# Kernel optimization log

Hardware: AMD Instinct MI355X
Metric: run time of the kernel (lower is better)

## Reference

```python
import jax, jax.numpy as jnp
import numpy as np

B, N, C, H = 2, 2048, 1024, 16
D = C // H
EPS = 1e-5  # torch LayerNorm default


def layernorm(x, gamma, beta):
    mu = jnp.mean(x, axis=-1, keepdims=True)
    var = jnp.mean(jnp.square(x - mu), axis=-1, keepdims=True)
    return (x - mu) * jax.lax.rsqrt(var + EPS) * gamma + beta


def setup_inputs() -> dict:
    key = jax.random.key(0)
    ks = jax.random.split(key, 4)
    x = jax.random.normal(ks[0], (B, N, C), dtype=jnp.float32)
    w_qkv = jax.random.normal(ks[1], (3 * C, C), dtype=jnp.float32) * (C ** -0.5)
    w_proj = jax.random.normal(ks[2], (C, C), dtype=jnp.float32) * (C ** -0.5)
    return {
        "x": x,
        "w_qkv": w_qkv,
        "q_gamma": jnp.ones((C,), jnp.float32),
        "q_beta": jnp.zeros((C,), jnp.float32),
        "k_gamma": jnp.ones((C,), jnp.float32),
        "k_beta": jnp.zeros((C,), jnp.float32),
        "lpe_w": jnp.ones((C,), jnp.float32),
        "lpe_b": jnp.zeros((C,), jnp.float32),
        "w_proj": w_proj,
        "b_proj": jnp.zeros((C,), jnp.float32),
    }


def reference(x, w_qkv, q_gamma, q_beta, k_gamma, k_beta, lpe_w, lpe_b, w_proj, b_proj):
    b, n, c = x.shape
    scale = D ** -0.5
    qkv = jnp.einsum('bnc,fc->bnf', x, w_qkv)            # (B,N,3C)
    qkv = qkv.reshape(b, n, 3, H, D)
    q, k, v = qkv[:, :, 0], qkv[:, :, 1], qkv[:, :, 2]   # (B,N,H,D)
    # QK-norm: LayerNorm over flattened heads (dim C)
    q = layernorm(q.reshape(b, n, c), q_gamma, q_beta).reshape(b, n, H, D)
    k = layernorm(k.reshape(b, n, c), k_gamma, k_beta).reshape(b, n, H, D)
    # LPE: depthwise 1x1x1 conv == per-channel affine on v
    v_lpe = v.reshape(b, n, c) * lpe_w + lpe_b           # (B,N,C)
    # attention
    attn = jnp.einsum('bqhd,bkhd->bhqk', q * scale, k)   # (B,H,N,N)
    attn = jax.nn.softmax(attn, axis=-1)
    out = jnp.einsum('bhqk,bkhd->bqhd', attn, v).reshape(b, n, c)
    y = jnp.einsum('bnc,oc->bno', out + v_lpe, w_proj) + b_proj
    return y
```

## Files before the change

kernel.cpp:

```cpp
#include <hip/hip_runtime.h>
#include <stdint.h>

#define Bdim 2
#define Ndim 2048
#define Cdim 1024
#define Hdim 16
#define Ddim 64
#define Fdim 3072
#define Mdim 4096

typedef unsigned int  u32;
typedef unsigned short u16;
typedef float f32x4 __attribute__((ext_vector_type(4)));
typedef short s16x8 __attribute__((ext_vector_type(8)));
typedef unsigned short u16x4 __attribute__((ext_vector_type(4)));
typedef unsigned int u32x2 __attribute__((ext_vector_type(2)));

__device__ __forceinline__ u16 f2b(float f) {
  u32 u = __builtin_bit_cast(u32, f);
  u += 0x7FFFu + ((u >> 16) & 1u);
  return (u16)(u >> 16);
}
__device__ __forceinline__ float b2f(u16 h) {
  return __builtin_bit_cast(float, (u32)h << 16);
}
__device__ __forceinline__ u32 cvtpk(float a, float b) {
  u32 d;
  asm("v_cvt_pk_bf16_f32 %0, %1, %2" : "=v"(d) : "v"(a), "v"(b));
  return d;
}
__device__ __forceinline__ float rexp2(float x) { return __builtin_amdgcn_exp2f(x); }
__device__ __forceinline__ f32x4 mfma16(s16x8 a, s16x8 b, f32x4 c) {
  return __builtin_amdgcn_mfma_f32_16x16x32_bf16(a, b, c, 0, 0, 0);
}
__device__ __forceinline__ void gl_lds16(const void* g, void* l) {
  __builtin_amdgcn_global_load_lds(
      (const __attribute__((address_space(1))) void*)g,
      (__attribute__((address_space(3))) void*)l, 16, 0, 0);
}
__device__ __forceinline__ bool is_bf16(const void* qg) {
  return *(const u32*)qg == 0x3F803F80u;
}

__global__ __launch_bounds__(256)
void k_prep(const void* x, const void* wq, const void* wp,
            const void* g0, const void* g1, const void* g2, const void* g3,
            const void* g4, const void* g5, const void* g6,
            u16* xb, u16* wqb, u16* wpb, float* prm) {
  const int i = blockIdx.x * 256 + threadIdx.x;
  const bool isbf = is_bf16(g0);
  const void* src; u16* dst; int k;
  if (i < 1048576)      { src = x;  dst = xb;  k = i; }
  else if (i < 1835008) { src = wq; dst = wqb; k = i - 1048576; }
  else if (i < 2097152) { src = wp; dst = wpb; k = i - 1835008; }
  else {
    const int j = i - 2097152;
    if (j >= 1792) return;
    const int fi = j * 4;
    const int pi = fi >> 10, off = fi & 1023;
    const void* s = (pi == 0) ? g0 : (pi == 1) ? g1 : (pi == 2) ? g2
                  : (pi == 3) ? g3 : (pi == 4) ? g4 : (pi == 5) ? g5 : g6;
    float4 v;
    if (isbf) {
      u16x4 h = *(const u16x4*)((const u16*)s + off);
      v.x = b2f(h.x); v.y = b2f(h.y); v.z = b2f(h.z); v.w = b2f(h.w);
    } else {
      v = *(const float4*)((const float*)s + off);
    }
    *(float4*)(prm + fi) = v;
    return;
  }
  if (isbf) {
    ((u16x4*)dst)[k] = ((const u16x4*)src)[k];
  } else {
    float4 v = ((const float4*)src)[k];
    u16x4 o;
    o.x = f2b(v.x); o.y = f2b(v.y); o.z = f2b(v.z); o.w = f2b(v.w);
    ((u16x4*)dst)[k] = o;
  }
}

template <int EPI>
__global__ __launch_bounds__(256)
void k_gemm_bt(const u16* __restrict__ A, const u16* __restrict__ W,
               u16* __restrict__ Cb, void* __restrict__ Cout,
               u16* __restrict__ vTp,
               const float* __restrict__ bias, const void* __restrict__ qg,
               int Msz, int Nsz, int Ksz) {
  __shared__ __align__(16) char lds[32768];
  const int tid = threadIdx.x;
  const int lane = tid & 63;
  const int wm = (tid >> 6) >> 1, wn = (tid >> 6) & 1;
  const int g = lane >> 4, cl = lane & 15;
  const int row0 = blockIdx.y * 128, col0 = blockIdx.x * 128;
  const int KT = Ksz >> 5;

  f32x4 acc[4][4] = {};

  auto stage = [&](int buf, int kt) {
    const int k0 = kt << 5;
#pragma unroll
    for (int iss = 0; iss < 2; ++iss) {
      const int t = iss * 256 + tid;
      const int r = t >> 2;
      const int ss = (t & 3) ^ ((r >> 1) & 3);
      gl_lds16(A + (size_t)(row0 + r) * Ksz + k0 + ss * 8, &lds[buf * 16384 + t * 16]);
      gl_lds16(W + (size_t)(col0 + r) * Ksz + k0 + ss * 8, &lds[buf * 16384 + 8192 + t * 16]);
    }
  };

  stage(0, 0);
  __syncthreads();
  int cur = 0;
  for (int kt = 0; kt < KT; ++kt) {
    if (kt + 1 < KT) stage(cur ^ 1, kt + 1);
    const char* Ab = &lds[cur * 16384];
    const char* Bb = &lds[cur * 16384 + 8192];
    s16x8 af[4], bfr[4];
#pragma unroll
    for (int mi = 0; mi < 4; ++mi) {
      const int r = wm * 64 + mi * 16 + cl;
      const int s = g ^ ((r >> 1) & 3);
      af[mi] = *(const s16x8*)(Ab + r * 64 + s * 16);
    }
#pragma unroll
    for (int nj = 0; nj < 4; ++nj) {
      const int r = wn * 64 + nj * 16 + cl;
      const int s = g ^ ((r >> 1) & 3);
      bfr[nj] = *(const s16x8*)(Bb + r * 64 + s * 16);
    }
#pragma unroll
    for (int mi = 0; mi < 4; ++mi)
#pragma unroll
      for (int nj = 0; nj < 4; ++nj)
        acc[mi][nj] = mfma16(af[mi], bfr[nj], acc[mi][nj]);
    __syncthreads();
    cur ^= 1;
  }

  const u32 oflag = (EPI == 1) ? (is_bf16(qg) ? 1u : 0u) : 0u;
#pragma unroll
  for (int mi = 0; mi < 4; ++mi)
#pragma unroll
    for (int nj = 0; nj < 4; ++nj) {
      const int m0 = row0 + wm * 64 + mi * 16 + g * 4;
      const int nbase = col0 + wn * 64 + nj * 16;
      const int n = nbase + cl;
      if (EPI == 2 && nbase >= 2048) {
        const int h = (nbase - 2048) >> 6;
        const int d = ((nbase - 2048) & 63) + cl;
        u16x4 pk;
#pragma unroll
        for (int r = 0; r < 4; ++r) pk[r] = f2b(acc[mi][nj][r]);
        *(u16x4*)(vTp + (size_t)h * (64 * 4096) + (size_t)d * 4096 + m0) = pk;
      } else {
#pragma unroll
        for (int r = 0; r < 4; ++r) {
          const int m = m0 + r;
          float v = acc[mi][nj][r];
          if (EPI == 2) {
            Cb[(size_t)m * Nsz + n] = f2b(v);
          } else {
            v += bias[n];
            if (oflag) ((u16*)Cout)[(size_t)m * Nsz + n] = f2b(v);
            else       ((float*)Cout)[(size_t)m * Nsz + n] = v;
          }
        }
      }
    }
}

__global__ __launch_bounds__(256)
void k_ln(u16* __restrict__ qkv, const float* __restrict__ prm) {
  const int m = blockIdx.x;
  const int tid = threadIdx.x;
  const int lane = tid & 63, wv = tid >> 6;
  __shared__ float red[2][4];
  u16* row = qkv + (size_t)m * Fdim;
#pragma unroll
  for (int seg = 0; seg < 2; ++seg) {
    u16* s = row + seg * 1024;
    u16x4 v = *(const u16x4*)(s + tid * 4);
    float x0 = b2f(v.x), x1 = b2f(v.y), x2 = b2f(v.z), x3 = b2f(v.w);
    float sum = x0 + x1 + x2 + x3;
    float ssq = x0 * x0 + x1 * x1 + x2 * x2 + x3 * x3;
#pragma unroll
    for (int off = 32; off >= 1; off >>= 1) {
      sum += __shfl_xor(sum, off);
      ssq += __shfl_xor(ssq, off);
    }
    if (lane == 0) { red[0][wv] = sum; red[1][wv] = ssq; }
    __syncthreads();
    const float ts = red[0][0] + red[0][1] + red[0][2] + red[0][3];
    const float tq = red[1][0] + red[1][1] + red[1][2] + red[1][3];
    __syncthreads();
    const float mu = ts * (1.0f / 1024.0f);
    const float var = tq * (1.0f / 1024.0f) - mu * mu;
    const float rstd = rsqrtf(var + 1e-5f);
    const float scl = (seg == 0) ? (0.125f * 1.4426950408889634f) : 1.0f;
    const float* gam = prm + seg * 2048;
    const float* bet = prm + seg * 2048 + 1024;
    const int c = tid * 4;
    u16x4 o;
    o.x = f2b(((x0 - mu) * rstd * gam[c + 0] + bet[c + 0]) * scl);
    o.y = f2b(((x1 - mu) * rstd * gam[c + 1] + bet[c + 1]) * scl);
    o.z = f2b(((x2 - mu) * rstd * gam[c + 2] + bet[c + 2]) * scl);
    o.w = f2b(((x3 - mu) * rstd * gam[c + 3] + bet[c + 3]) * scl);
    *(u16x4*)(s + tid * 4) = o;
  }
}

__global__ __launch_bounds__(256, 3)
void k_attn(const u16* __restrict__ qkv, const u16* __restrict__ vT,
            u16* __restrict__ pin, const float* __restrict__ prm) {
  const int bid = blockIdx.x;
  const int qt = (bid >> 3) & 15;
  const int bh = (bid & 7) * 4 + (bid >> 7);
  const int b = bh >> 4, h = bh & 15;
  const int tid = threadIdx.x, lane = tid & 63, w = tid >> 6;
  const int g = lane >> 4, cl = lane & 15;
  const int c7 = cl & 7;
  const int mrow0 = b * Ndim + qt * 128;
  const int NT = Ndim / 64;

  const u16* Qg  = qkv + (size_t)mrow0 * Fdim + h * 64;
  const u16* Kg  = qkv + (size_t)(b * Ndim) * Fdim + Cdim + h * 64;
  const u16* vTg = vT + (size_t)h * (64 * 4096) + b * Ndim;

  __shared__ __align__(16) char klds[2][8192];
  __shared__ __align__(16) char vlds[2][8192];
  __shared__ __align__(16) char plds[4][4096];

  s16x8 bq[2][2];
#pragma unroll
  for (int qb = 0; qb < 2; ++qb)
#pragma unroll
    for (int kc = 0; kc < 2; ++kc)
      bq[qb][kc] = *(const s16x8*)(Qg + (size_t)(w * 32 + qb * 16 + cl) * Fdim + kc * 32 + g * 8);

  f32x4 o[2][4] = {};
  float mr[2] = {-1e30f, -1e30f};
  float lr[2] = {0.f, 0.f};

  const char* akp0 = &klds[0][cl * 128 + (((0 + g) ^ c7) << 4)];
  const char* akp1 = &klds[0][cl * 128 + (((4 + g) ^ c7) << 4)];
  const char* avp0 = &vlds[0][cl * 128 + (((0 + g) ^ c7) << 4)];
  const char* avp1 = &vlds[0][cl * 128 + (((4 + g) ^ c7) << 4)];
  char* pwp[4];
#pragma unroll
  for (int nj = 0; nj < 4; ++nj)
    pwp[nj] = &plds[w][cl * 128 + ((nj * 32 + g * 8) ^ (c7 << 4))];
  const char* bpp0 = &plds[w][cl * 128 + ((0  + g * 16) ^ (c7 << 4))];
  const char* bpp1 = &plds[w][cl * 128 + ((64 + g * 16) ^ (c7 << 4))];

  const int r0 = tid >> 3;
  const int ss0 = ((tid & 7) ^ (r0 & 7)) * 8;
  const u16* kp = Kg + (size_t)r0 * Fdim + ss0;
  const u16* vp = vTg + (size_t)r0 * 4096 + ss0;
  char* kd = &klds[0][tid * 16];
  char* vd = &vlds[0][tid * 16];

  gl_lds16(kp, kd);
  gl_lds16(kp + (size_t)32 * Fdim, kd + 4096);
  gl_lds16(vp, vd);
  gl_lds16(vp + (size_t)32 * 4096, vd + 4096);
  kp += (size_t)64 * Fdim;
  vp += 64;

#define ATTN_TILE(BUF, PREFETCH)                                              \
  {                                                                           \
               \
    asm volatile("s_waitcnt vmcnt(2)" ::: "memory");                          \
    __builtin_amdgcn_s_barrier();                                             \
    __builtin_amdgcn_sched_barrier(0);                                        \
    if (PREFETCH) {                                                           \
      gl_lds16(kp, kd + ((BUF) ^ 1) * 8192);                                  \
      gl_lds16(kp + (size_t)32 * Fdim, kd + ((BUF) ^ 1) * 8192 + 4096);       \
      gl_lds16(vp, vd + ((BUF) ^ 1) * 8192);                                  \
      gl_lds16(vp + (size_t)32 * 4096, vd + ((BUF) ^ 1) * 8192 + 4096);       \
      kp += (size_t)64 * Fdim;                                                \
      vp += 64;                                                               \
    }                                                                         \
    s16x8 ak[4][2];                                                           \
    _Pragma("unroll") for (int nj = 0; nj < 4; ++nj) {                        \
      ak[nj][0] = *(const s16x8*)(akp0 + (BUF) * 8192 + nj * 2048);           \
      ak[nj][1] = *(const s16x8*)(akp1 + (BUF) * 8192 + nj * 2048);           \
    }                                                                         \
    _Pragma("unroll") for (int qb = 0; qb < 2; ++qb) {                        \
      f32x4 sv[4];                                                            \
      __builtin_amdgcn_s_setprio(1);                                          \
      _Pragma("unroll") for (int nj = 0; nj < 4; ++nj) {                      \
        f32x4 z = {0.f, 0.f, 0.f, 0.f};                                       \
        z = mfma16(ak[nj][0], bq[qb][0], z);                                  \
        z = mfma16(ak[nj][1], bq[qb][1], z);                                  \
        sv[nj] = z;                                                           \
      }                                                                       \
      __builtin_amdgcn_s_setprio(0);                                          \
      float a0 = fmaxf(fmaxf(sv[0][0], sv[0][1]), sv[0][2]);                  \
      float a1 = fmaxf(fmaxf(sv[0][3], sv[1][0]), sv[1][1]);                  \
      float a2 = fmaxf(fmaxf(sv[1][2], sv[1][3]), sv[2][0]);                  \
      float a3 = fmaxf(fmaxf(sv[2][1], sv[2][2]), sv[2][3]);                  \
      float a4 = fmaxf(fmaxf(sv[3][0], sv[3][1]), sv[3][2]);                  \
      float b0v = fmaxf(fmaxf(a0, a1), a2);                                   \
      float b1v = fmaxf(fmaxf(a3, a4), sv[3][3]);                             \
      float mx = fmaxf(b0v, b1v);                                             \
      if (!__all(mx <= mr[qb] + 7.0f)) {                                      \
        mx = fmaxf(mx, __shfl_xor(mx, 16));                                   \
        mx = fmaxf(mx, __shfl_xor(mx, 32));                                   \
        const float mn = fmaxf(mr[qb], mx);                                   \
        const float corr = rexp2(mr[qb] - mn);                                \
        mr[qb] = mn;                                                          \
        lr[qb] *= corr;                                                       \
        o[qb][0] *= corr; o[qb][1] *= corr;                                   \
        o[qb][2] *= corr; o[qb][3] *= corr;                                   \
      }                                                                       \
      const float mrq = mr[qb];                                               \
      float ssum = 0.f;                                                       \
      _Pragma("unroll") for (int nj = 0; nj < 4; ++nj) {                      \
        const float p0 = rexp2(sv[nj][0] - mrq), p1 = rexp2(sv[nj][1] - mrq); \
        const float p2 = rexp2(sv[nj][2] - mrq), p3 = rexp2(sv[nj][3] - mrq); \
        ssum += (p0 + p1) + (p2 + p3);                                        \
        u32x2 pk2;                                                            \
        pk2.x = cvtpk(p0, p1);                                                \
        pk2.y = cvtpk(p2, p3);                                                \
        *(u32x2*)(pwp[nj] + qb * 2048) = pk2;                                 \
      }                                                                       \
      lr[qb] += ssum;                                                         \
    }                                                                         \
           \
    if (PREFETCH) {                                                           \
      asm volatile("s_waitcnt vmcnt(4) lgkmcnt(0)" ::: "memory");             \
    } else {                                                                  \
      asm volatile("s_waitcnt vmcnt(0) lgkmcnt(0)" ::: "memory");             \
    }                                                                         \
    __builtin_amdgcn_s_barrier();                                             \
    __builtin_amdgcn_sched_barrier(0);                                        \
    s16x8 av[4][2];                                                           \
    _Pragma("unroll") for (int dc = 0; dc < 4; ++dc) {                        \
      av[dc][0] = *(const s16x8*)(avp0 + (BUF) * 8192 + dc * 2048);           \
      av[dc][1] = *(const s16x8*)(avp1 + (BUF) * 8192 + dc * 2048);           \
    }                                                                         \
    _Pragma("unroll") for (int qb = 0; qb < 2; ++qb) {                        \
      const s16x8 bp0 = *(const s16x8*)(bpp0 + qb * 2048);                    \
      const s16x8 bp1 = *(const s16x8*)(bpp1 + qb * 2048);                    \
      __builtin_amdgcn_s_setprio(1);                                          \
      _Pragma("unroll") for (int dc = 0; dc < 4; ++dc) {                      \
        o[qb][dc] = mfma16(av[dc][0], bp0, o[qb][dc]);                        \
        o[qb][dc] = mfma16(av[dc][1], bp1, o[qb][dc]);                        \
      }                                                                       \
      __builtin_amdgcn_s_setprio(0);                                          \
    }                                                                         \
  }

  for (int t = 0; t < NT; t += 2) {
    ATTN_TILE(0, true);
    ATTN_TILE(1, (t + 2 < NT));
  }
#undef ATTN_TILE

#pragma unroll
  for (int qb = 0; qb < 2; ++qb) {
    const int q = w * 32 + qb * 16 + cl;
    const int m = mrow0 + q;
    const int nseq = qt * 128 + q;
    float lt = lr[qb];
    lt += __shfl_xor(lt, 16);
    lt += __shfl_xor(lt, 32);
    const float inv = 1.0f / lt;
#pragma unroll
    for (int dc = 0; dc < 4; ++dc) {
      const int d0 = dc * 16 + g * 4;
      const int c = h * 64 + d0;
      const float4 lw = *(const float4*)(prm + 4096 + c);
      const float4 lb = *(const float4*)(prm + 5120 + c);
      float vr[4];
#pragma unroll
      for (int r = 0; r < 4; ++r) {
        const float vv = b2f(vTg[(size_t)(d0 + r) * 4096 + nseq]);
        vr[r] = o[qb][dc][r] * inv + vv * (&lw.x)[r] + (&lb.x)[r];
      }
      u32x2 ov;
      ov.x = cvtpk(vr[0], vr[1]);
      ov.y = cvtpk(vr[2], vr[3]);
      *(u32x2*)(pin + (size_t)m * Cdim + c) = ov;
    }
  }
}

extern "C" void kernel_launch(void* const* d_in, const int* in_sizes, int n_in,
                              void* d_out, int out_size, void* d_ws, size_t ws_size,
                              hipStream_t stream) {
  (void)in_sizes; (void)n_in; (void)out_size; (void)ws_size;
  char* ws = (char*)d_ws;
  float* prm    = (float*)(ws + 256);
  u16*   xb     = (u16*)(ws + 32768);
  u16*   wqkvb  = (u16*)(ws + 32768 + 8388608);
  u16*   wprojb = (u16*)(ws + 32768 + 8388608 + 6291456);
  u16*   qkv    = (u16*)(ws + 32768 + 8388608 + 6291456 + 2097152);
  u16*   vT     = (u16*)(ws + 32768 + 8388608 + 6291456 + 2097152 + 25165824);
  u16*   pin    = xb;

  k_prep<<<8199, 256, 0, stream>>>(d_in[0], d_in[1], d_in[8],
                                   d_in[2], d_in[3], d_in[4], d_in[5],
                                   d_in[6], d_in[7], d_in[9],
                                   xb, wqkvb, wprojb, prm);

  k_gemm_bt<2><<<dim3(Fdim / 128, Mdim / 128), 256, 0, stream>>>(
      xb, wqkvb, qkv, nullptr, vT, nullptr, nullptr, Mdim, Fdim, Cdim);

  k_ln<<<Mdim, 256, 0, stream>>>(qkv, prm);

  k_attn<<<dim3(512), 256, 0, stream>>>(qkv, vT, pin, prm);

  k_gemm_bt<1><<<dim3(Cdim / 128, Mdim / 128), 256, 0, stream>>>(
      pin, wprojb, nullptr, d_out, nullptr, prm + 6144, d_in[2], Mdim, Cdim, Cdim);
}
```

Measured before the change: 134.9 us.

## Load K and V fragments directly from global into registers, dropping LDS staging

The attention kernel no longer stages K and V tiles through double-buffered shared memory with block barriers. Each wave now loads its own K and V MFMA fragments straight from global memory into registers, keeping a register double buffer for K and loading V at the start of each tile. The launch-bounds occupancy hint is also dropped. This removes the LDS round trip and the per-tile barriers, but each of the four waves now fetches the same K/V data redundantly, which increases global/L2 traffic and register pressure.

After: 199.3 us. 1.48x slower.

```diff
diff --git a/kernel.cpp b/kernel.cpp
--- a/kernel.cpp
+++ b/kernel.cpp
@@ -210,7 +210,7 @@
   }
 }
 
-__global__ __launch_bounds__(256, 3)
+__global__ __launch_bounds__(256)
 void k_attn(const u16* __restrict__ qkv, const u16* __restrict__ vT,
             u16* __restrict__ pin, const float* __restrict__ prm) {
   const int bid = blockIdx.x;
@@ -227,8 +227,6 @@
   const u16* Kg  = qkv + (size_t)(b * Ndim) * Fdim + Cdim + h * 64;
   const u16* vTg = vT + (size_t)h * (64 * 4096) + b * Ndim;
 
-  __shared__ __align__(16) char klds[2][8192];
-  __shared__ __align__(16) char vlds[2][8192];
   __shared__ __align__(16) char plds[4][4096];
 
   s16x8 bq[2][2];
@@ -242,10 +240,6 @@
   float mr[2] = {-1e30f, -1e30f};
   float lr[2] = {0.f, 0.f};
 
-  const char* akp0 = &klds[0][cl * 128 + (((0 + g) ^ c7) << 4)];
-  const char* akp1 = &klds[0][cl * 128 + (((4 + g) ^ c7) << 4)];
-  const char* avp0 = &vlds[0][cl * 128 + (((0 + g) ^ c7) << 4)];
-  const char* avp1 = &vlds[0][cl * 128 + (((4 + g) ^ c7) << 4)];
   char* pwp[4];
 #pragma unroll
   for (int nj = 0; nj < 4; ++nj)
@@ -253,46 +247,39 @@
   const char* bpp0 = &plds[w][cl * 128 + ((0  + g * 16) ^ (c7 << 4))];
   const char* bpp1 = &plds[w][cl * 128 + ((64 + g * 16) ^ (c7 << 4))];
 
-  const int r0 = tid >> 3;
-  const int ss0 = ((tid & 7) ^ (r0 & 7)) * 8;
-  const u16* kp = Kg + (size_t)r0 * Fdim + ss0;
-  const u16* vp = vTg + (size_t)r0 * 4096 + ss0;
-  char* kd = &klds[0][tid * 16];
-  char* vd = &vlds[0][tid * 16];
-
-  gl_lds16(kp, kd);
-  gl_lds16(kp + (size_t)32 * Fdim, kd + 4096);
-  gl_lds16(vp, vd);
-  gl_lds16(vp + (size_t)32 * 4096, vd + 4096);
-  kp += (size_t)64 * Fdim;
-  vp += 64;
-
-#define ATTN_TILE(BUF, PREFETCH)                                              \
+  const u16* kt_p = Kg + (size_t)cl * Fdim + g * 8;
+  const u16* vt_p = vTg + (size_t)cl * 4096 + g * 8;
+
+  s16x8 kA[4][2], kB[4][2];
+#pragma unroll
+  for (int nj = 0; nj < 4; ++nj)
+#pragma unroll
+    for (int kc = 0; kc < 2; ++kc)
+      kA[nj][kc] = *(const s16x8*)(kt_p + (size_t)(nj * 16) * Fdim + kc * 32);
+  kt_p += (size_t)64 * Fdim;
+
+#define ATTN_TILE(KTHIS, KNEXT, PREFETCH)                                     \
   {                                                                           \
-               \
-    asm volatile("s_waitcnt vmcnt(2)" ::: "memory");                          \
-    __builtin_amdgcn_s_barrier();                                             \
-    __builtin_amdgcn_sched_barrier(0);                                        \
+                           \
+    s16x8 vr[4][2];                                                           \
+    _Pragma("unroll") for (int dc = 0; dc < 4; ++dc)                          \
+      _Pragma("unroll") for (int ks = 0; ks < 2; ++ks)                        \
+        vr[dc][ks] = *(const s16x8*)(vt_p + (size_t)(dc * 16) * 4096 + ks * 32); \
+    vt_p += 64;                                                               \
+                                \
     if (PREFETCH) {                                                           \
-      gl_lds16(kp, kd + ((BUF) ^ 1) * 8192);                                  \
-      gl_lds16(kp + (size_t)32 * Fdim, kd + ((BUF) ^ 1) * 8192 + 4096);       \
-      gl_lds16(vp, vd + ((BUF) ^ 1) * 8192);                                  \
-      gl_lds16(vp + (size_t)32 * 4096, vd + ((BUF) ^ 1) * 8192 + 4096);       \
-      kp += (size_t)64 * Fdim;                                                \
-      vp += 64;                                                               \
-    }                                                                         \
-    s16x8 ak[4][2];                                                           \
-    _Pragma("unroll") for (int nj = 0; nj < 4; ++nj) {                        \
-      ak[nj][0] = *(const s16x8*)(akp0 + (BUF) * 8192 + nj * 2048);           \
-      ak[nj][1] = *(const s16x8*)(akp1 + (BUF) * 8192 + nj * 2048);           \
+      _Pragma("unroll") for (int nj = 0; nj < 4; ++nj)                        \
+        _Pragma("unroll") for (int kc = 0; kc < 2; ++kc)                      \
+          KNEXT[nj][kc] = *(const s16x8*)(kt_p + (size_t)(nj * 16) * Fdim + kc * 32); \
+      kt_p += (size_t)64 * Fdim;                                              \
     }                                                                         \
     _Pragma("unroll") for (int qb = 0; qb < 2; ++qb) {                        \
       f32x4 sv[4];                                                            \
       __builtin_amdgcn_s_setprio(1);                                          \
       _Pragma("unroll") for (int nj = 0; nj < 4; ++nj) {                      \
         f32x4 z = {0.f, 0.f, 0.f, 0.f};                                       \
-        z = mfma16(ak[nj][0], bq[qb][0], z);                                  \
-        z = mfma16(ak[nj][1], bq[qb][1], z);                                  \
+        z = mfma16(KTHIS[nj][0], bq[qb][0], z);                               \
+        z = mfma16(KTHIS[nj][1], bq[qb][1], z);                               \
         sv[nj] = z;                                                           \
       }                                                                       \
       __builtin_amdgcn_s_setprio(0);                                          \
@@ -327,34 +314,24 @@
       }                                                                       \
       lr[qb] += ssum;                                                         \
     }                                                                         \
-           \
-    if (PREFETCH) {                                                           \
-      asm volatile("s_waitcnt vmcnt(4) lgkmcnt(0)" ::: "memory");             \
-    } else {                                                                  \
-      asm volatile("s_waitcnt vmcnt(0) lgkmcnt(0)" ::: "memory");             \
-    }                                                                         \
-    __builtin_amdgcn_s_barrier();                                             \
+     \
+    asm volatile("s_waitcnt lgkmcnt(0)" ::: "memory");                        \
     __builtin_amdgcn_sched_barrier(0);                                        \
-    s16x8 av[4][2];                                                           \
-    _Pragma("unroll") for (int dc = 0; dc < 4; ++dc) {                        \
-      av[dc][0] = *(const s16x8*)(avp0 + (BUF) * 8192 + dc * 2048);           \
-      av[dc][1] = *(const s16x8*)(avp1 + (BUF) * 8192 + dc * 2048);           \
-    }                                                                         \
     _Pragma("unroll") for (int qb = 0; qb < 2; ++qb) {                        \
       const s16x8 bp0 = *(const s16x8*)(bpp0 + qb * 2048);                    \
       const s16x8 bp1 = *(const s16x8*)(bpp1 + qb * 2048);                    \
       __builtin_amdgcn_s_setprio(1);                                          \
       _Pragma("unroll") for (int dc = 0; dc < 4; ++dc) {                      \
-        o[qb][dc] = mfma16(av[dc][0], bp0, o[qb][dc]);                        \
-        o[qb][dc] = mfma16(av[dc][1], bp1, o[qb][dc]);                        \
+        o[qb][dc] = mfma16(vr[dc][0], bp0, o[qb][dc]);                        \
+        o[qb][dc] = mfma16(vr[dc][1], bp1, o[qb][dc]);                        \
       }                                                                       \
       __builtin_amdgcn_s_setprio(0);                                          \
     }                                                                         \
   }
 
   for (int t = 0; t < NT; t += 2) {
-    ATTN_TILE(0, true);
-    ATTN_TILE(1, (t + 2 < NT));
+    ATTN_TILE(kA, kB, true);
+    ATTN_TILE(kB, kA, (t + 2 < NT));
   }
 #undef ATTN_TILE
 
@@ -373,15 +350,15 @@
       const int c = h * 64 + d0;
       const float4 lw = *(const float4*)(prm + 4096 + c);
       const float4 lb = *(const float4*)(prm + 5120 + c);
-      float vr[4];
+      float vr2[4];
 #pragma unroll
       for (int r = 0; r < 4; ++r) {
         const float vv = b2f(vTg[(size_t)(d0 + r) * 4096 + nseq]);
-        vr[r] = o[qb][dc][r] * inv + vv * (&lw.x)[r] + (&lb.x)[r];
+        vr2[r] = o[qb][dc][r] * inv + vv * (&lw.x)[r] + (&lb.x)[r];
       }
       u32x2 ov;
-      ov.x = cvtpk(vr[0], vr[1]);
-      ov.y = cvtpk(vr[2], vr[3]);
+      ov.x = cvtpk(vr2[0], vr2[1]);
+      ov.y = cvtpk(vr2[2], vr2[3]);
       *(u32x2*)(pin + (size_t)m * Cdim + c) = ov;
     }
   }
```
